# Kernel tuning notes

Hardware: AMD Instinct MI355X
Metric: run time of the kernel (lower is better)

## Reference

```python
import jax, jax.numpy as jnp
import numpy as np

T, B, D, H = 512, 128, 512, 512


def setup_inputs() -> dict:
    key = jax.random.key(0)
    ks = jax.random.split(key, 6)
    scale = 0.05
    ins = jax.random.normal(ks[0], (T, B, D), dtype=jnp.float32)
    resets = jax.random.randint(ks[1], (T, B), 0, 2).astype(jnp.bool_)
    h0 = jnp.zeros((B, H), dtype=jnp.float32)
    # input kernels for r,z,n concatenated: [D, 3H]
    Wi = jax.random.normal(ks[2], (D, 3 * H), dtype=jnp.float32) * scale
    bi = jnp.zeros((3 * H,), dtype=jnp.float32)
    # recurrent kernels: hr,hz (no bias) concatenated [H, 2H]; hn [H, H] with bias
    Wh_rz = jax.random.normal(ks[3], (H, 2 * H), dtype=jnp.float32) * scale
    Wh_n = jax.random.normal(ks[4], (H, H), dtype=jnp.float32) * scale
    bh_n = jnp.zeros((H,), dtype=jnp.float32)
    return {"ins": ins, "resets": resets, "h0": h0, "Wi": Wi, "bi": bi,
            "Wh_rz": Wh_rz, "Wh_n": Wh_n, "bh_n": bh_n}


def reference(ins, resets, h0, Wi, bi, Wh_rz, Wh_n, bh_n):
    # Precompute input projections for all timesteps (same math, hoisted GEMM)
    x_proj = jnp.einsum('tbd,dk->tbk', ins, Wi) + bi  # [T, B, 3H]

    def step(h, xs):
        xp, rst = xs  # xp: [B, 3H], rst: [B]
        # reset-masked carry: zero the hidden state where reset flag is set
        h = jnp.where(rst[:, None], 0.0, h)
        xr, xz, xn = jnp.split(xp, 3, axis=-1)
        hr, hz = jnp.split(h @ Wh_rz, 2, axis=-1)
        r = jax.nn.sigmoid(xr + hr)
        z = jax.nn.sigmoid(xz + hz)
        n = jnp.tanh(xn + r * (h @ Wh_n + bh_n))
        h_new = (1.0 - z) * n + z * h
        return h_new, h_new  # GRUCell returns (carry, y) with y == carry

    hT, ys = jax.lax.scan(step, h0, (x_proj, resets))
    return hT, ys
```

## Files before the change

kernel.cpp:

```cpp
#include <hip/hip_runtime.h>

typedef unsigned short u16;
typedef unsigned int u32;
typedef unsigned long long u64;
typedef short short8 __attribute__((ext_vector_type(8)));
typedef float f32x4 __attribute__((ext_vector_type(4)));

static constexpr int T = 512, B = 128, D = 512, H = 512;

static constexpr size_t WS_WPACK = 0;
static constexpr size_t WS_MASK  = 3145728;
static constexpr size_t WS_HBF   = WS_MASK + 262144;
static constexpr size_t WS_FLAGS = WS_HBF + 262144;
static constexpr size_t WS_XBF   = WS_FLAGS + 1024;

__device__ __forceinline__ u32 f2bf(float f) {
  unsigned b = __float_as_uint(f);
  b = (b + 0x7FFFu + ((b >> 16) & 1u)) >> 16;
  return b & 0xFFFFu;
}

__global__ void pack_w_kernel(const float* __restrict__ Wi,
                              const float* __restrict__ Whrz,
                              const float* __restrict__ Whn,
                              u16* __restrict__ wpack) {
  int c = blockIdx.x * 256 + threadIdx.x;
  if (c >= 32 * 128 * 48) return;
  int n  = c % 48;
  int kb = (c / 48) % 128;
  int cgrp = c / (48 * 128);
  int g = n >> 4, jl = n & 15;
  int j = cgrp * 16 + jl;
  u16 tmp[8] __attribute__((aligned(16)));
#pragma unroll
  for (int i = 0; i < 8; ++i) {
    int k = kb * 8 + i;
    float v;
    if (k < 512) {
      v = Wi[k * 1536 + g * 512 + j];
    } else {
      int kh = k - 512;
      v = (g == 0) ? Whrz[kh * 1024 + j]
        : (g == 1) ? Whrz[kh * 1024 + 512 + j]
                   : Whn[kh * 512 + j];
    }
    tmp[i] = (u16)f2bf(v);
  }
  *reinterpret_cast<uint4*>(wpack + (size_t)c * 8) = *reinterpret_cast<const uint4*>(tmp);
}

__global__ void init_kernel(const void* __restrict__ resets_raw,
                            const float* __restrict__ h0,
                            float* __restrict__ mask,
                            u16* __restrict__ hbf,
                            u32* __restrict__ flags) {
  __shared__ int s_flags;
  if (threadIdx.x == 0) s_flags = 0;
  __syncthreads();
  const unsigned char* u8 = (const unsigned char*)resets_raw;
  {
    int p = threadIdx.x * 4;
    int f = 0;
    if (u8[p + 1] | u8[p + 2]) f |= 1;
    unsigned char b3 = u8[p + 3];
    if (b3 == 0x3F) f |= 2;
    else if (b3) f |= 1;
    if (f) atomicOr(&s_flags, f);
  }
  __syncthreads();
  int flags_d = s_flags;
  int idx = blockIdx.x * 256 + threadIdx.x;
  bool rv;
  if (flags_d & 2)      rv = ((const float*)resets_raw)[idx] != 0.0f;
  else if (flags_d & 1) rv = u8[idx] != 0;
  else                  rv = ((const int*)resets_raw)[idx] != 0;
  mask[idx] = rv ? 0.0f : 1.0f;
  int b = idx >> 9;
  bool r0;
  if (flags_d & 2)      r0 = ((const float*)resets_raw)[b] != 0.0f;
  else if (flags_d & 1) r0 = u8[b] != 0;
  else                  r0 = ((const int*)resets_raw)[b] != 0;
  float h = r0 ? 0.0f : h0[idx];
  hbf[idx] = (u16)f2bf(h);
  if (blockIdx.x == 0 && threadIdx.x < 256) flags[threadIdx.x] = 0;
}

__global__ void convert_x_kernel(const float* __restrict__ ins, u16* __restrict__ xbf) {
  size_t i = ((size_t)blockIdx.x * 256 + threadIdx.x) * 8;
  float4 f0 = *reinterpret_cast<const float4*>(ins + i);
  float4 f1 = *reinterpret_cast<const float4*>(ins + i + 4);
  u16 tmp[8] __attribute__((aligned(16)));
  tmp[0] = (u16)f2bf(f0.x); tmp[1] = (u16)f2bf(f0.y);
  tmp[2] = (u16)f2bf(f0.z); tmp[3] = (u16)f2bf(f0.w);
  tmp[4] = (u16)f2bf(f1.x); tmp[5] = (u16)f2bf(f1.y);
  tmp[6] = (u16)f2bf(f1.z); tmp[7] = (u16)f2bf(f1.w);
  *reinterpret_cast<uint4*>(xbf + i) = *reinterpret_cast<const uint4*>(tmp);
}

__launch_bounds__(256, 1)
__global__ void scan_kernel(const float* __restrict__ ins,
                            const u16* __restrict__ xbf,
                            const float* __restrict__ h0,
                            const float* __restrict__ bi,
                            const float* __restrict__ bhn,
                            const u16* __restrict__ wpack,
                            const float* __restrict__ mask,
                            u16* __restrict__ hbf,
                            u32* __restrict__ flags,
                            float* __restrict__ out) {
  extern __shared__ char smem[];
  u16*   w_lds = (u16*)smem;
  float* o_lds = (float*)(smem + 98304);

  const int tid  = threadIdx.x;
  const int rg   = blockIdx.x & 7;
  const int cgi  = blockIdx.x >> 3;
  const int lane = tid & 63;
  const int wv   = tid >> 6;
  const int quad = lane >> 4;
  const int lm   = lane & 15;

  {
    const u16* src = wpack + (size_t)cgi * (128 * 48 * 8);
    for (int o = tid; o < 128 * 48; o += 256)
      *reinterpret_cast<uint4*>(w_lds + o * 8) = *reinterpret_cast<const uint4*>(src + o * 8);
  }

  const int nb  = (wv == 3) ? 32 : wv * 16;
  const int row = rg * 16 + lm;
  const int b_l = tid >> 4, j_l = tid & 15;
  const int b_g = rg * 16 + b_l;
  const int j_g = cgi * 16 + j_l;
  const float bi_r = bi[j_g], bi_z = bi[512 + j_g], bi_n = bi[1024 + j_g];
  const float bh_nv = bhn[j_g];
  float* ys = out + (size_t)B * H;

  float hprev = h0[b_g * H + j_g];
  float mcur  = mask[b_g];

  const u64* hbf64 = (const u64*)hbf;
  u32*       hbf32 = (u32*)hbf;

  __syncthreads();

  for (int t = 0; t < T; ++t) {
    const int buf = t & 1;
    f32x4 acc = {0.f, 0.f, 0.f, 0.f};

    if (wv != 3) {
      if (xbf) {
        const u16* xs = xbf + ((size_t)t * B + row) * D;
#pragma unroll
        for (int kk = 0; kk < 16; ++kk) {
          int kb = kk * 4 + quad;
          short8 av = *reinterpret_cast<const short8*>(xs + kb * 8);
          short8 bv = *reinterpret_cast<const short8*>(w_lds + (kb * 48 + nb + lm) * 8);
          acc = __builtin_amdgcn_mfma_f32_16x16x32_bf16(av, bv, acc, 0, 0, 0);
        }
      } else {
        const float* xs = ins + ((size_t)t * B + row) * D;
#pragma unroll
        for (int kk = 0; kk < 16; ++kk) {
          int kb = kk * 4 + quad;
          float4 f0 = *reinterpret_cast<const float4*>(xs + kb * 8);
          float4 f1 = *reinterpret_cast<const float4*>(xs + kb * 8 + 4);
          u16 tmp[8] __attribute__((aligned(16)));
          tmp[0] = (u16)f2bf(f0.x); tmp[1] = (u16)f2bf(f0.y);
          tmp[2] = (u16)f2bf(f0.z); tmp[3] = (u16)f2bf(f0.w);
          tmp[4] = (u16)f2bf(f1.x); tmp[5] = (u16)f2bf(f1.y);
          tmp[6] = (u16)f2bf(f1.z); tmp[7] = (u16)f2bf(f1.w);
          short8 av = *reinterpret_cast<const short8*>(tmp);
          short8 bv = *reinterpret_cast<const short8*>(w_lds + (kb * 48 + nb + lm) * 8);
          acc = __builtin_amdgcn_mfma_f32_16x16x32_bf16(av, bv, acc, 0, 0, 0);
        }
      }
    }

    if (t) {
      const u32* fp = flags + rg * 32 + (lane & 31);
      while (true) {
        u32 f = __hip_atomic_load(fp, __ATOMIC_RELAXED, __HIP_MEMORY_SCOPE_AGENT);
        if (__all((int)(f >= (u32)t))) break;
      }
    }

    if (wv != 2) {
      const size_t hb = ((size_t)buf * B + row) * 128;
#pragma unroll
      for (int kk = 16; kk < 32; ++kk) {
        int kb = kk * 4 + quad;
        union { u64 d[2]; short8 v; } hu;
        const u64* hp = hbf64 + hb + (size_t)(kb - 64) * 2;
        hu.d[0] = __hip_atomic_load(hp,     __ATOMIC_RELAXED, __HIP_MEMORY_SCOPE_AGENT);
        hu.d[1] = __hip_atomic_load(hp + 1, __ATOMIC_RELAXED, __HIP_MEMORY_SCOPE_AGENT);
        short8 bv = *reinterpret_cast<const short8*>(w_lds + (kb * 48 + nb + lm) * 8);
        acc = __builtin_amdgcn_mfma_f32_16x16x32_bf16(hu.v, bv, acc, 0, 0, 0);
      }
    }
#pragma unroll
    for (int r = 0; r < 4; ++r)
      o_lds[wv * 256 + (quad * 4 + r) * 16 + lm] = acc[r];
    __syncthreads();

    float racc = o_lds[      b_l * 16 + j_l] + bi_r;
    float zacc = o_lds[256 + b_l * 16 + j_l] + bi_z;
    float xnv  = o_lds[512 + b_l * 16 + j_l] + bi_n;
    float hnv  = o_lds[768 + b_l * 16 + j_l] + bh_nv;
    float hp = hprev * mcur;
    float rr = 1.0f / (1.0f + __expf(-racc));
    float zz = 1.0f / (1.0f + __expf(-zacc));
    float nn = tanhf(xnv + rr * hnv);
    float hnew = (1.0f - zz) * nn + zz * hp;
    ys[((size_t)t * B + b_g) * H + j_g] = hnew;
    float mnext = (t < T - 1) ? mask[(t + 1) * B + b_g] : 1.0f;
    u32 mybf  = f2bf(hnew * mnext);
    u32 other = (u32)__shfl_xor((int)mybf, 1);
    if (!(j_l & 1)) {
      u32 packed = mybf | (other << 16);
      __hip_atomic_store(hbf32 + ((size_t)(1 - buf) * B + b_g) * 256 + (j_g >> 1),
                         packed, __ATOMIC_RELAXED, __HIP_MEMORY_SCOPE_AGENT);
    }
    if (t == T - 1) out[b_g * H + j_g] = hnew;
    hprev = hnew; mcur = mnext;
    __syncthreads();
    if (t < T - 1 && tid == 0)
      __hip_atomic_store(flags + rg * 32 + cgi, (u32)(t + 1),
                         __ATOMIC_RELEASE, __HIP_MEMORY_SCOPE_AGENT);
  }
}

extern "C" void kernel_launch(void* const* d_in, const int* in_sizes, int n_in,
                              void* d_out, int out_size, void* d_ws, size_t ws_size,
                              hipStream_t stream) {
  const float* ins  = (const float*)d_in[0];
  const void*  rst  = d_in[1];
  const float* h0   = (const float*)d_in[2];
  const float* Wi   = (const float*)d_in[3];
  const float* bi   = (const float*)d_in[4];
  const float* Whrz = (const float*)d_in[5];
  const float* Whn  = (const float*)d_in[6];
  const float* bhn  = (const float*)d_in[7];

  char* ws = (char*)d_ws;
  u16*   wpack = (u16*)(ws + WS_WPACK);
  float* mask  = (float*)(ws + WS_MASK);
  u16*   hbf   = (u16*)(ws + WS_HBF);
  u32*   flags = (u32*)(ws + WS_FLAGS);
  float* out   = (float*)d_out;

  bool big = ws_size >= WS_XBF + (size_t)T * B * D * 2;
  const u16* xbf = big ? (const u16*)(ws + WS_XBF) : nullptr;

  hipLaunchKernelGGL(pack_w_kernel, dim3(768), dim3(256), 0, stream, Wi, Whrz, Whn, wpack);
  hipLaunchKernelGGL(init_kernel, dim3(256), dim3(256), 0, stream, rst, h0, mask, hbf, flags);
  if (big)
    hipLaunchKernelGGL(convert_x_kernel, dim3(16384), dim3(256), 0, stream,
                       ins, (u16*)(ws + WS_XBF));

  (void)hipFuncSetAttribute((const void*)scan_kernel,
                            hipFuncAttributeMaxDynamicSharedMemorySize, 102400);
  void* args[10];
  args[0] = (void*)&ins;   args[1] = (void*)&xbf;  args[2] = (void*)&h0;
  args[3] = (void*)&bi;    args[4] = (void*)&bhn;  args[5] = (void*)&wpack;
  args[6] = (void*)&mask;  args[7] = (void*)&hbf;  args[8] = (void*)&flags;
  args[9] = (void*)&out;
  (void)hipLaunchCooperativeKernel((const void*)scan_kernel, dim3(256), dim3(256),
                                   args, 102400, stream);
}
```

Before: 4.106 ms.

## Keep weights in registers, pack h/x in MFMA layout, stage h via LDS

Weights move from LDS into per-wave registers (breg). The hidden state and the bf16 inputs are written in an MFMA-fragment layout so each load is contiguous. One wave waits on the flags, loads h into LDS once for the whole block, and the other waves read it from LDS. Flags become per-wave, dropping the trailing block barrier, and tanh is replaced by an exp-based formula. Together these aim to cut global-load latency and sync on the serial critical path, at the cost of heavy register pressure and an extra LDS barrier per step.

```diff
diff --git a/kernel.cpp b/kernel.cpp
--- a/kernel.cpp
+++ b/kernel.cpp
@@ -10,9 +10,9 @@
 
 static constexpr size_t WS_WPACK = 0;
 static constexpr size_t WS_MASK  = 3145728;
-static constexpr size_t WS_HBF   = WS_MASK + 262144;
-static constexpr size_t WS_FLAGS = WS_HBF + 262144;
-static constexpr size_t WS_XBF   = WS_FLAGS + 1024;
+static constexpr size_t WS_HBFA  = WS_MASK + 262144;
+static constexpr size_t WS_FLAGS = WS_HBFA + 262144;
+static constexpr size_t WS_XPACK = WS_FLAGS + 4096;
 
 __device__ __forceinline__ u32 f2bf(float f) {
   unsigned b = __float_as_uint(f);
@@ -52,7 +52,7 @@
 __global__ void init_kernel(const void* __restrict__ resets_raw,
                             const float* __restrict__ h0,
                             float* __restrict__ mask,
-                            u16* __restrict__ hbf,
+                            u16* __restrict__ hbfA,
                             u32* __restrict__ flags) {
   __shared__ int s_flags;
   if (threadIdx.x == 0) s_flags = 0;
@@ -68,49 +68,66 @@
     if (f) atomicOr(&s_flags, f);
   }
   __syncthreads();
-  int flags_d = s_flags;
+  int fl = s_flags;
   int idx = blockIdx.x * 256 + threadIdx.x;
   bool rv;
-  if (flags_d & 2)      rv = ((const float*)resets_raw)[idx] != 0.0f;
-  else if (flags_d & 1) rv = u8[idx] != 0;
-  else                  rv = ((const int*)resets_raw)[idx] != 0;
+  if (fl & 2)      rv = ((const float*)resets_raw)[idx] != 0.0f;
+  else if (fl & 1) rv = u8[idx] != 0;
+  else             rv = ((const int*)resets_raw)[idx] != 0;
   mask[idx] = rv ? 0.0f : 1.0f;
-  int b = idx >> 9;
+  int b = idx >> 9, j = idx & 511;
   bool r0;
-  if (flags_d & 2)      r0 = ((const float*)resets_raw)[b] != 0.0f;
-  else if (flags_d & 1) r0 = u8[b] != 0;
-  else                  r0 = ((const int*)resets_raw)[b] != 0;
+  if (fl & 2)      r0 = ((const float*)resets_raw)[b] != 0.0f;
+  else if (fl & 1) r0 = u8[b] != 0;
+  else             r0 = ((const int*)resets_raw)[b] != 0;
   float h = r0 ? 0.0f : h0[idx];
-  hbf[idx] = (u16)f2bf(h);
-  if (blockIdx.x == 0 && threadIdx.x < 256) flags[threadIdx.x] = 0;
-}
-
-__global__ void convert_x_kernel(const float* __restrict__ ins, u16* __restrict__ xbf) {
-  size_t i = ((size_t)blockIdx.x * 256 + threadIdx.x) * 8;
-  float4 f0 = *reinterpret_cast<const float4*>(ins + i);
-  float4 f1 = *reinterpret_cast<const float4*>(ins + i + 4);
-  u16 tmp[8] __attribute__((aligned(16)));
-  tmp[0] = (u16)f2bf(f0.x); tmp[1] = (u16)f2bf(f0.y);
-  tmp[2] = (u16)f2bf(f0.z); tmp[3] = (u16)f2bf(f0.w);
-  tmp[4] = (u16)f2bf(f1.x); tmp[5] = (u16)f2bf(f1.y);
-  tmp[6] = (u16)f2bf(f1.z); tmp[7] = (u16)f2bf(f1.w);
-  *reinterpret_cast<uint4*>(xbf + i) = *reinterpret_cast<const uint4*>(tmp);
+  int rg = b >> 4, row = b & 15, kb = j >> 3, i = j & 7;
+  hbfA[(((size_t)rg * 64 + kb) * 16 + row) * 8 + i] = (u16)f2bf(h);
+  if (blockIdx.x < 4) flags[blockIdx.x * 256 + threadIdx.x] = 0;
+}
+
+__global__ void convert_x_kernel(const float* __restrict__ ins, u16* __restrict__ xpack) {
+  __shared__ u16 s_x[16 * 520];
+  int t = blockIdx.x >> 3, rg = blockIdx.x & 7;
+  int tid = threadIdx.x;
+#pragma unroll
+  for (int p = 0; p < 4; ++p) {
+    int row = p * 4 + (tid >> 6);
+    int col = (tid & 63) * 8;
+    const float* s = ins + ((size_t)t * B + rg * 16 + row) * D + col;
+    float4 f0 = *reinterpret_cast<const float4*>(s);
+    float4 f1 = *reinterpret_cast<const float4*>(s + 4);
+    u16* d = s_x + row * 520 + col;
+    d[0]=(u16)f2bf(f0.x); d[1]=(u16)f2bf(f0.y); d[2]=(u16)f2bf(f0.z); d[3]=(u16)f2bf(f0.w);
+    d[4]=(u16)f2bf(f1.x); d[5]=(u16)f2bf(f1.y); d[6]=(u16)f2bf(f1.z); d[7]=(u16)f2bf(f1.w);
+  }
+  __syncthreads();
+  u16* dst = xpack + ((size_t)t * 8 + rg) * 8192;
+#pragma unroll
+  for (int p = 0; p < 4; ++p) {
+    int f = p * 256 + tid;
+    int kb = f >> 4, row = f & 15;
+    const u16* sp = s_x + row * 520 + kb * 8;
+    u16 tmp[8] __attribute__((aligned(16)));
+#pragma unroll
+    for (int i = 0; i < 8; ++i) tmp[i] = sp[i];
+    *reinterpret_cast<uint4*>(dst + (size_t)f * 8) = *reinterpret_cast<const uint4*>(tmp);
+  }
 }
 
 __launch_bounds__(256, 1)
 __global__ void scan_kernel(const float* __restrict__ ins,
-                            const u16* __restrict__ xbf,
+                            const u16* __restrict__ xpack,
                             const float* __restrict__ h0,
                             const float* __restrict__ bi,
                             const float* __restrict__ bhn,
                             const u16* __restrict__ wpack,
                             const float* __restrict__ mask,
-                            u16* __restrict__ hbf,
+                            u16* __restrict__ hbfA,
                             u32* __restrict__ flags,
                             float* __restrict__ out) {
-  extern __shared__ char smem[];
-  u16*   w_lds = (u16*)smem;
-  float* o_lds = (float*)(smem + 98304);
+  __shared__ u16  a_lds[64 * 16 * 8];
+  __shared__ float o_lds[4 * 256];
 
   const int tid  = threadIdx.x;
   const int rg   = blockIdx.x & 7;
@@ -120,14 +137,27 @@
   const int quad = lane >> 4;
   const int lm   = lane & 15;
 
+  short8 breg[32];
   {
-    const u16* src = wpack + (size_t)cgi * (128 * 48 * 8);
-    for (int o = tid; o < 128 * 48; o += 256)
-      *reinterpret_cast<uint4*>(w_lds + o * 8) = *reinterpret_cast<const uint4*>(src + o * 8);
-  }
-
-  const int nb  = (wv == 3) ? 32 : wv * 16;
-  const int row = rg * 16 + lm;
+    const u16* wp = wpack + (size_t)cgi * (128 * 48 * 8);
+    if (wv < 2) {
+      int n = wv * 16 + lm;
+#pragma unroll
+      for (int kk = 0; kk < 32; ++kk) {
+        int kb = kk * 4 + quad;
+        breg[kk] = *reinterpret_cast<const short8*>(wp + ((size_t)kb * 48 + n) * 8);
+      }
+    } else {
+      int n = 32 + lm;
+      int kbb = (wv == 2) ? 64 : 0;
+#pragma unroll
+      for (int kk = 0; kk < 16; ++kk) {
+        int kb = kbb + kk * 4 + quad;
+        breg[kk] = *reinterpret_cast<const short8*>(wp + ((size_t)kb * 48 + n) * 8);
+      }
+    }
+  }
+
   const int b_l = tid >> 4, j_l = tid & 15;
   const int b_g = rg * 16 + b_l;
   const int j_g = cgi * 16 + j_l;
@@ -137,64 +167,72 @@
 
   float hprev = h0[b_g * H + j_g];
   float mcur  = mask[b_g];
-
-  const u64* hbf64 = (const u64*)hbf;
-  u32*       hbf32 = (u32*)hbf;
-
-  __syncthreads();
+  const int kb_st = cgi * 2 + (j_l >> 3);
+  u32* hbfA32 = (u32*)hbfA;
 
   for (int t = 0; t < T; ++t) {
     const int buf = t & 1;
+    float mnext = (t < T - 1) ? mask[(t + 1) * B + b_g] : 1.0f;
     f32x4 acc = {0.f, 0.f, 0.f, 0.f};
 
-    if (wv != 3) {
-      if (xbf) {
-        const u16* xs = xbf + ((size_t)t * B + row) * D;
+    if (wv != 2) {
+      if (xpack) {
+        const u16* xs = xpack + ((size_t)t * 8 + rg) * 8192;
 #pragma unroll
         for (int kk = 0; kk < 16; ++kk) {
           int kb = kk * 4 + quad;
-          short8 av = *reinterpret_cast<const short8*>(xs + kb * 8);
-          short8 bv = *reinterpret_cast<const short8*>(w_lds + (kb * 48 + nb + lm) * 8);
-          acc = __builtin_amdgcn_mfma_f32_16x16x32_bf16(av, bv, acc, 0, 0, 0);
+          short8 av = *reinterpret_cast<const short8*>(xs + ((size_t)kb * 16 + lm) * 8);
+          acc = __builtin_amdgcn_mfma_f32_16x16x32_bf16(av, breg[kk], acc, 0, 0, 0);
         }
       } else {
-        const float* xs = ins + ((size_t)t * B + row) * D;
+        const float* xs = ins + ((size_t)t * B + rg * 16 + lm) * D;
 #pragma unroll
         for (int kk = 0; kk < 16; ++kk) {
           int kb = kk * 4 + quad;
           float4 f0 = *reinterpret_cast<const float4*>(xs + kb * 8);
           float4 f1 = *reinterpret_cast<const float4*>(xs + kb * 8 + 4);
           u16 tmp[8] __attribute__((aligned(16)));
-          tmp[0] = (u16)f2bf(f0.x); tmp[1] = (u16)f2bf(f0.y);
-          tmp[2] = (u16)f2bf(f0.z); tmp[3] = (u16)f2bf(f0.w);
-          tmp[4] = (u16)f2bf(f1.x); tmp[5] = (u16)f2bf(f1.y);
-          tmp[6] = (u16)f2bf(f1.z); tmp[7] = (u16)f2bf(f1.w);
+          tmp[0]=(u16)f2bf(f0.x); tmp[1]=(u16)f2bf(f0.y); tmp[2]=(u16)f2bf(f0.z); tmp[3]=(u16)f2bf(f0.w);
+          tmp[4]=(u16)f2bf(f1.x); tmp[5]=(u16)f2bf(f1.y); tmp[6]=(u16)f2bf(f1.z); tmp[7]=(u16)f2bf(f1.w);
           short8 av = *reinterpret_cast<const short8*>(tmp);
-          short8 bv = *reinterpret_cast<const short8*>(w_lds + (kb * 48 + nb + lm) * 8);
-          acc = __builtin_amdgcn_mfma_f32_16x16x32_bf16(av, bv, acc, 0, 0, 0);
+          acc = __builtin_amdgcn_mfma_f32_16x16x32_bf16(av, breg[kk], acc, 0, 0, 0);
         }
       }
-    }
-
-    if (t) {
-      const u32* fp = flags + rg * 32 + (lane & 31);
-      while (true) {
-        u32 f = __hip_atomic_load(fp, __ATOMIC_RELAXED, __HIP_MEMORY_SCOPE_AGENT);
-        if (__all((int)(f >= (u32)t))) break;
-      }
-    }
-
-    if (wv != 2) {
-      const size_t hb = ((size_t)buf * B + row) * 128;
+    } else {
+      if (t) {
+        const u64* fp = (const u64*)(flags + rg * 128);
+        while (true) {
+          u64 f = __hip_atomic_load(fp + lane, __ATOMIC_RELAXED, __HIP_MEMORY_SCOPE_AGENT);
+          if (__all(((u32)f >= (u32)t) && ((u32)(f >> 32) >= (u32)t))) break;
+        }
+      }
+      const u64* src = (const u64*)(hbfA + ((size_t)buf * 8 + rg) * 8192);
+      union HU { u64 d[2]; short8 v; } hu[16];
+#pragma unroll
+      for (int c = 0; c < 16; ++c) {
+        const u64* p = src + c * 128 + lane * 2;
+        hu[c].d[0] = __hip_atomic_load(p,     __ATOMIC_RELAXED, __HIP_MEMORY_SCOPE_AGENT);
+        hu[c].d[1] = __hip_atomic_load(p + 1, __ATOMIC_RELAXED, __HIP_MEMORY_SCOPE_AGENT);
+      }
+#pragma unroll
+      for (int c = 0; c < 16; ++c)
+        *reinterpret_cast<short8*>(a_lds + ((size_t)c * 64 + lane) * 8) = hu[c].v;
+    }
+    __syncthreads();
+
+    if (wv < 2) {
 #pragma unroll
       for (int kk = 16; kk < 32; ++kk) {
-        int kb = kk * 4 + quad;
-        union { u64 d[2]; short8 v; } hu;
-        const u64* hp = hbf64 + hb + (size_t)(kb - 64) * 2;
-        hu.d[0] = __hip_atomic_load(hp,     __ATOMIC_RELAXED, __HIP_MEMORY_SCOPE_AGENT);
-        hu.d[1] = __hip_atomic_load(hp + 1, __ATOMIC_RELAXED, __HIP_MEMORY_SCOPE_AGENT);
-        short8 bv = *reinterpret_cast<const short8*>(w_lds + (kb * 48 + nb + lm) * 8);
-        acc = __builtin_amdgcn_mfma_f32_16x16x32_bf16(hu.v, bv, acc, 0, 0, 0);
+        int kbh = (kk - 16) * 4 + quad;
+        short8 av = *reinterpret_cast<const short8*>(a_lds + ((size_t)kbh * 16 + lm) * 8);
+        acc = __builtin_amdgcn_mfma_f32_16x16x32_bf16(av, breg[kk], acc, 0, 0, 0);
+      }
+    } else if (wv == 2) {
+#pragma unroll
+      for (int kk = 0; kk < 16; ++kk) {
+        int kbh = kk * 4 + quad;
+        short8 av = *reinterpret_cast<const short8*>(a_lds + ((size_t)kbh * 16 + lm) * 8);
+        acc = __builtin_amdgcn_mfma_f32_16x16x32_bf16(av, breg[kk], acc, 0, 0, 0);
       }
     }
 #pragma unroll
@@ -204,27 +242,26 @@
 
     float racc = o_lds[      b_l * 16 + j_l] + bi_r;
     float zacc = o_lds[256 + b_l * 16 + j_l] + bi_z;
-    float xnv  = o_lds[512 + b_l * 16 + j_l] + bi_n;
-    float hnv  = o_lds[768 + b_l * 16 + j_l] + bh_nv;
+    float hnv  = o_lds[512 + b_l * 16 + j_l] + bh_nv;
+    float xnv  = o_lds[768 + b_l * 16 + j_l] + bi_n;
     float hp = hprev * mcur;
     float rr = 1.0f / (1.0f + __expf(-racc));
     float zz = 1.0f / (1.0f + __expf(-zacc));
-    float nn = tanhf(xnv + rr * hnv);
+    float s  = xnv + rr * hnv;
+    float nn = 1.0f - 2.0f / (1.0f + __expf(2.0f * s));
     float hnew = (1.0f - zz) * nn + zz * hp;
     ys[((size_t)t * B + b_g) * H + j_g] = hnew;
-    float mnext = (t < T - 1) ? mask[(t + 1) * B + b_g] : 1.0f;
     u32 mybf  = f2bf(hnew * mnext);
     u32 other = (u32)__shfl_xor((int)mybf, 1);
     if (!(j_l & 1)) {
-      u32 packed = mybf | (other << 16);
-      __hip_atomic_store(hbf32 + ((size_t)(1 - buf) * B + b_g) * 256 + (j_g >> 1),
-                         packed, __ATOMIC_RELAXED, __HIP_MEMORY_SCOPE_AGENT);
+      size_t o32 = (((size_t)(1 - buf) * 8 + rg) * 64 + kb_st) * 64 + b_l * 4 + ((j_l & 7) >> 1);
+      __hip_atomic_store(hbfA32 + o32, mybf | (other << 16),
+                         __ATOMIC_RELAXED, __HIP_MEMORY_SCOPE_AGENT);
     }
     if (t == T - 1) out[b_g * H + j_g] = hnew;
     hprev = hnew; mcur = mnext;
-    __syncthreads();
-    if (t < T - 1 && tid == 0)
-      __hip_atomic_store(flags + rg * 32 + cgi, (u32)(t + 1),
+    if (t < T - 1 && lane == 0)
+      __hip_atomic_store(flags + rg * 128 + cgi * 4 + wv, (u32)(t + 1),
                          __ATOMIC_RELEASE, __HIP_MEMORY_SCOPE_AGENT);
   }
 }
@@ -244,26 +281,24 @@
   char* ws = (char*)d_ws;
   u16*   wpack = (u16*)(ws + WS_WPACK);
   float* mask  = (float*)(ws + WS_MASK);
-  u16*   hbf   = (u16*)(ws + WS_HBF);
+  u16*   hbfA  = (u16*)(ws + WS_HBFA);
   u32*   flags = (u32*)(ws + WS_FLAGS);
   float* out   = (float*)d_out;
 
-  bool big = ws_size >= WS_XBF + (size_t)T * B * D * 2;
-  const u16* xbf = big ? (const u16*)(ws + WS_XBF) : nullptr;
+  bool big = ws_size >= WS_XPACK + (size_t)T * B * D * 2;
+  const u16* xpack = big ? (const u16*)(ws + WS_XPACK) : nullptr;
 
   hipLaunchKernelGGL(pack_w_kernel, dim3(768), dim3(256), 0, stream, Wi, Whrz, Whn, wpack);
-  hipLaunchKernelGGL(init_kernel, dim3(256), dim3(256), 0, stream, rst, h0, mask, hbf, flags);
+  hipLaunchKernelGGL(init_kernel, dim3(256), dim3(256), 0, stream, rst, h0, mask, hbfA, flags);
   if (big)
-    hipLaunchKernelGGL(convert_x_kernel, dim3(16384), dim3(256), 0, stream,
-                       ins, (u16*)(ws + WS_XBF));
-
-  (void)hipFuncSetAttribute((const void*)scan_kernel,
-                            hipFuncAttributeMaxDynamicSharedMemorySize, 102400);
+    hipLaunchKernelGGL(convert_x_kernel, dim3(4096), dim3(256), 0, stream,
+                       ins, (u16*)(ws + WS_XPACK));
+
   void* args[10];
-  args[0] = (void*)&ins;   args[1] = (void*)&xbf;  args[2] = (void*)&h0;
-  args[3] = (void*)&bi;    args[4] = (void*)&bhn;  args[5] = (void*)&wpack;
-  args[6] = (void*)&mask;  args[7] = (void*)&hbf;  args[8] = (void*)&flags;
+  args[0] = (void*)&ins;   args[1] = (void*)&xpack; args[2] = (void*)&h0;
+  args[3] = (void*)&bi;    args[4] = (void*)&bhn;   args[5] = (void*)&wpack;
+  args[6] = (void*)&mask;  args[7] = (void*)&hbfA;  args[8] = (void*)&flags;
   args[9] = (void*)&out;
   (void)hipLaunchCooperativeKernel((const void*)scan_kernel, dim3(256), dim3(256),
-                                   args, 102400, stream);
-}
+                                   args, 0, stream);
+}
```

Result: slower. 8.531 ms (+107.7%).
